# Kernel optimization log

Measured on AMD Instinct MI355X. Metric: run time of the kernel, lower is better.

The kernel has to match this reference:

```python
import jax, jax.numpy as jnp
import numpy as np

EMBED_DIM = 1024
NUM_HEADS = 16
HEAD_DIM = EMBED_DIM // NUM_HEADS


def setup_inputs() -> dict:
    key = jax.random.key(0)
    ks = jax.random.split(key, 5)
    T, B, E = 2048, 2, EMBED_DIM
    s = 1.0 / np.sqrt(E)
    return {
        "x": jax.random.normal(ks[0], (T, B, E), jnp.float32),
        "wq": jax.random.normal(ks[1], (E, E), jnp.float32) * s,
        "bq": jnp.zeros((E,), jnp.float32),
        "wk": jax.random.normal(ks[2], (E, E), jnp.float32) * s,
        "bk": jnp.zeros((E,), jnp.float32),
        "wv": jax.random.normal(ks[3], (E, E), jnp.float32) * s,
        "bv": jnp.zeros((E,), jnp.float32),
        "wo": jax.random.normal(ks[4], (E, E), jnp.float32) * s,
        "bo": jnp.zeros((E,), jnp.float32),
    }


def reference(x, wq, bq, wk, bk, wv, bv, wo, bo):
    # x: [T, B, E] (Time x Batch x Channel), self-attention: query = key = value = x
    T, B, E = x.shape
    H, D = NUM_HEADS, HEAD_DIM
    scaling = D ** -0.5
    # Linear projections (torch Linear: y = x @ W.T + b)
    q = (jnp.einsum('tbe,fe->tbf', x, wq) + bq) * scaling
    k = jnp.einsum('tbe,fe->tbf', x, wk) + bk
    v = jnp.einsum('tbe,fe->tbf', x, wv) + bv
    # reshape to [B*H, T, D] equivalent -> use [B, H, T, D]
    q = q.reshape(T, B, H, D).transpose(1, 2, 0, 3)  # [B,H,T,D]
    k = k.reshape(T, B, H, D).transpose(1, 2, 0, 3)
    v = v.reshape(T, B, H, D).transpose(1, 2, 0, 3)
    # scores: [B,H,T,S], fp32 softmax
    scores = jnp.einsum('bhtd,bhsd->bhts', q, k)
    probs = jax.nn.softmax(scores.astype(jnp.float32), axis=-1).astype(x.dtype)
    attn = jnp.einsum('bhts,bhsd->bhtd', probs, v)  # [B,H,T,D]
    attn = attn.transpose(2, 0, 1, 3).reshape(T, B, E)
    out = jnp.einsum('tbe,fe->tbf', attn, wo) + bo
    return out
```

## Files before the change

### kernel.cpp

```cpp
#include <hip/hip_runtime.h>
#include <cstddef>
#include <cstdint>

#define T_DIM 2048
#define E_DIM 1024
#define M_DIM 4096

typedef __attribute__((ext_vector_type(8))) short short8;
typedef __attribute__((ext_vector_type(8))) _Float16 half8;
typedef __attribute__((ext_vector_type(4))) float f32x4;

__device__ __forceinline__ short f16_bits(float v) {
  return __builtin_bit_cast(short, (_Float16)v);
}
__device__ __forceinline__ unsigned int pk2(float a, float b) {
  return __builtin_bit_cast(unsigned int, __builtin_amdgcn_cvt_pkrtz(a, b));
}
__device__ __forceinline__ half8 h8(short8 s) { return __builtin_bit_cast(half8, s); }

__device__ __forceinline__ void gl_lds16(const short* g, const short* l) {
  __builtin_amdgcn_global_load_lds(
      (const __attribute__((address_space(1))) unsigned int*)g,
      (__attribute__((address_space(3))) unsigned int*)l, 16, 0, 0);
}

__global__ __launch_bounds__(256) void convert_all(
    const float* __restrict__ x, const float* __restrict__ wq,
    const float* __restrict__ wk, const float* __restrict__ wv,
    const float* __restrict__ wo,
    short* __restrict__ xh, short* __restrict__ wqh, short* __restrict__ wkh,
    short* __restrict__ wvh, short* __restrict__ woh)
{
  const int bid = blockIdx.x;
  const float* in; short* hi; int base;
  if (bid < 4096)      { in = x;  hi = xh;  base = 0;    }
  else if (bid < 5120) { in = wq; hi = wqh; base = 4096; }
  else if (bid < 6144) { in = wk; hi = wkh; base = 5120; }
  else if (bid < 7168) { in = wv; hi = wvh; base = 6144; }
  else                 { in = wo; hi = woh; base = 7168; }
  const int i = (bid - base) * 256 + threadIdx.x;
  float4 v = ((const float4*)in)[i];
  uint2 p;
  p.x = (unsigned short)f16_bits(v.x) | ((unsigned int)(unsigned short)f16_bits(v.y) << 16);
  p.y = (unsigned short)f16_bits(v.z) | ((unsigned int)(unsigned short)f16_bits(v.w) << 16);
  ((uint2*)hi)[i] = p;
}

__global__ __launch_bounds__(256) void gemm_qkv(
    const short* __restrict__ xh,
    const short* __restrict__ wqh, const short* __restrict__ wkh,
    const short* __restrict__ wvh,
    const float* __restrict__ bq, const float* __restrict__ bk,
    const float* __restrict__ bv,
    short* __restrict__ qo, short* __restrict__ ko, short* __restrict__ vto)
{
  __shared__ __align__(16) short Ah[128 * 32], Wh[128 * 32];
  const int tid = threadIdx.x;
  const int lane = tid & 63;
  const int w = tid >> 6;
  const int quad = lane >> 4;
  const int l15 = lane & 15;
  const int sel = blockIdx.x >> 3;
  const int n0 = (blockIdx.x & 7) * 128;
  const int m0 = blockIdx.y * 128;

  const short* wsel = sel == 0 ? wqh : sel == 1 ? wkh : wvh;
  const float* bias = sel == 0 ? bq : sel == 1 ? bk : bv;
  const float scale = sel == 0 ? 0.125f * 1.44269504088896f : 1.0f;

  const short* gsrc = (w < 2) ? xh : wsel;
  short* lbuf = (w < 2) ? Ah : Wh;
  const int rbase = (w < 2) ? m0 : n0;
  const int jb = (w & 1) * 4;
  const int lrow = lane >> 2;
  const int gphys = lane & 3;

  f32x4 zero = {0.f, 0.f, 0.f, 0.f};
  f32x4 acc[4][4];
#pragma unroll
  for (int i = 0; i < 4; ++i)
#pragma unroll
    for (int j = 0; j < 4; ++j) acc[i][j] = zero;

  const int wm = w & 1, wn = w >> 1;

  for (int k0 = 0; k0 < E_DIM; k0 += 32) {
    __syncthreads();
#pragma unroll
    for (int jj = 0; jj < 4; ++jj) {
      int j = jb + jj;
      int r = j * 16 + lrow;
      int gl = (gphys - (r >> 1)) & 3;
      gl_lds16(gsrc + (size_t)(rbase + r) * E_DIM + k0 + gl * 8, lbuf + j * 512);
    }
    __syncthreads();
    short8 ahf[4];
#pragma unroll
    for (int i = 0; i < 4; ++i) {
      int r = wm * 64 + i * 16 + l15;
      int idx = r * 32 + ((quad + (r >> 1)) & 3) * 8;
      ahf[i] = *(const short8*)&Ah[idx];
    }
#pragma unroll
    for (int j = 0; j < 4; ++j) {
      int r = wn * 64 + j * 16 + l15;
      int idx = r * 32 + ((quad + (r >> 1)) & 3) * 8;
      short8 bhf = *(const short8*)&Wh[idx];
#pragma unroll
      for (int i = 0; i < 4; ++i)
        acc[i][j] = __builtin_amdgcn_mfma_f32_16x16x32_f16(h8(ahf[i]), h8(bhf), acc[i][j], 0, 0, 0);
    }
  }

#pragma unroll
  for (int j = 0; j < 4; ++j) {
    const int gc = n0 + wn * 64 + j * 16 + l15;
    const float bb = bias[gc];
    const int h = gc >> 6, d = gc & 63;
#pragma unroll
    for (int i = 0; i < 4; ++i) {
#pragma unroll
      for (int reg = 0; reg < 4; ++reg) {
        const int gm = m0 + wm * 64 + i * 16 + quad * 4 + reg;
        const float val = (acc[i][j][reg] + bb) * scale;
        const int t = gm >> 1, b = gm & 1;
        if (sel < 2) {
          short* dst = sel == 0 ? qo : ko;
          dst[((size_t)(b * 16 + h) * T_DIM + t) * 64 + d] = f16_bits(val);
        } else {
          vto[((size_t)(b * 16 + h) * 64 + d) * T_DIM + t] = f16_bits(val);
        }
      }
    }
  }
}

__global__ __launch_bounds__(256) void gemm_out(
    const short* __restrict__ attn, const short* __restrict__ woh,
    const float* __restrict__ bo, float* __restrict__ out)
{
  __shared__ __align__(16) short Ah[128 * 32], Wh[128 * 32];
  const int tid = threadIdx.x;
  const int lane = tid & 63;
  const int w = tid >> 6;
  const int quad = lane >> 4;
  const int l15 = lane & 15;
  const int n0 = blockIdx.x * 128;
  const int m0 = blockIdx.y * 128;

  const short* gsrc = (w < 2) ? attn : woh;
  short* lbuf = (w < 2) ? Ah : Wh;
  const int rbase = (w < 2) ? m0 : n0;
  const int jb = (w & 1) * 4;
  const int lrow = lane >> 2;
  const int gphys = lane & 3;

  f32x4 zero = {0.f, 0.f, 0.f, 0.f};
  f32x4 acc[4][4];
#pragma unroll
  for (int i = 0; i < 4; ++i)
#pragma unroll
    for (int j = 0; j < 4; ++j) acc[i][j] = zero;

  const int wm = w & 1, wn = w >> 1;

  for (int k0 = 0; k0 < E_DIM; k0 += 32) {
    __syncthreads();
#pragma unroll
    for (int jj = 0; jj < 4; ++jj) {
      int j = jb + jj;
      int r = j * 16 + lrow;
      int gl = (gphys - (r >> 1)) & 3;
      gl_lds16(gsrc + (size_t)(rbase + r) * E_DIM + k0 + gl * 8, lbuf + j * 512);
    }
    __syncthreads();
    short8 ahf[4];
#pragma unroll
    for (int i = 0; i < 4; ++i) {
      int r = wm * 64 + i * 16 + l15;
      int idx = r * 32 + ((quad + (r >> 1)) & 3) * 8;
      ahf[i] = *(const short8*)&Ah[idx];
    }
#pragma unroll
    for (int j = 0; j < 4; ++j) {
      int r = wn * 64 + j * 16 + l15;
      int idx = r * 32 + ((quad + (r >> 1)) & 3) * 8;
      short8 bhf = *(const short8*)&Wh[idx];
#pragma unroll
      for (int i = 0; i < 4; ++i)
        acc[i][j] = __builtin_amdgcn_mfma_f32_16x16x32_f16(h8(ahf[i]), h8(bhf), acc[i][j], 0, 0, 0);
    }
  }

#pragma unroll
  for (int j = 0; j < 4; ++j) {
    const int gc = n0 + wn * 64 + j * 16 + l15;
    const float bb = bo[gc];
#pragma unroll
    for (int i = 0; i < 4; ++i)
#pragma unroll
      for (int reg = 0; reg < 4; ++reg) {
        const int gm = m0 + wm * 64 + i * 16 + quad * 4 + reg;
        out[(size_t)gm * E_DIM + gc] = acc[i][j][reg] + bb;
      }
  }
}

__global__ __launch_bounds__(256) void attn_mfma(
    const short* __restrict__ q, const short* __restrict__ k,
    const short* __restrict__ vt, short* __restrict__ attn)
{
  __shared__ __align__(16) short Qs[128 * 64], Ks[64 * 64], Vs[64 * 64], Ps[4 * 32 * 64];
  const int tid = threadIdx.x;
  const int lane = tid & 63;
  const int w = tid >> 6;
  const int quad = lane >> 4;
  const int l15 = lane & 15;
  const int bhid = blockIdx.y;
  const int b = bhid >> 4, h = bhid & 15;
  const int t0 = blockIdx.x * 128;

  const short* qb = q + (size_t)bhid * T_DIM * 64;
  const short* kb = k + (size_t)bhid * T_DIM * 64;
  const short* vb = vt + (size_t)bhid * 64 * T_DIM;

  const int lrow8 = lane >> 3;
  const int gph8 = lane & 7;

#pragma unroll
  for (int jj = 0; jj < 4; ++jj) {
    int j = w * 4 + jj;
    int r = j * 8 + lrow8;
    int gl = (gph8 - (r >> 1)) & 7;
    gl_lds16(qb + (size_t)(t0 + r) * 64 + gl * 8, Qs + j * 512);
  }

  f32x4 zero = {0.f, 0.f, 0.f, 0.f};
  f32x4 acc[2][4];
  float l_part[2] = {0.f, 0.f};
#pragma unroll
  for (int rb = 0; rb < 2; ++rb)
#pragma unroll
    for (int jd = 0; jd < 4; ++jd) acc[rb][jd] = zero;

  short8 qa[2][2];

  for (int s0 = 0; s0 < T_DIM; s0 += 64) {
    __syncthreads();
    {
      const short* sb = (w < 2) ? kb : vb;
      short* lb = (w < 2) ? Ks : Vs;
      const int jb = (w & 1) * 4;
#pragma unroll
      for (int jj = 0; jj < 4; ++jj) {
        int j = jb + jj;
        int r = j * 8 + lrow8;
        int gl = (gph8 - (r >> 1)) & 7;
        size_t goff = (w < 2) ? (size_t)(s0 + r) * 64 + gl * 8
                              : (size_t)r * T_DIM + s0 + gl * 8;
        gl_lds16(sb + goff, lb + j * 512);
      }
    }
    __syncthreads();

    if (s0 == 0) {
#pragma unroll
      for (int rb = 0; rb < 2; ++rb)
#pragma unroll
        for (int step = 0; step < 2; ++step) {
          int r = w * 32 + rb * 16 + l15;
          int idx = r * 64 + (((step * 4 + quad) + (r >> 1)) & 7) * 8;
          qa[rb][step] = *(const short8*)&Qs[idx];
        }
    }

    f32x4 sc[2][4];
#pragma unroll
    for (int rb = 0; rb < 2; ++rb)
#pragma unroll
      for (int j = 0; j < 4; ++j) sc[rb][j] = zero;
#pragma unroll
    for (int j = 0; j < 4; ++j) {
      short8 kf[2];
#pragma unroll
      for (int step = 0; step < 2; ++step) {
        int r = j * 16 + l15;
        int idx = r * 64 + (((step * 4 + quad) + (r >> 1)) & 7) * 8;
        kf[step] = *(const short8*)&Ks[idx];
      }
#pragma unroll
      for (int rb = 0; rb < 2; ++rb)
#pragma unroll
        for (int step = 0; step < 2; ++step)
          sc[rb][j] = __builtin_amdgcn_mfma_f32_16x16x32_f16(h8(kf[step]), h8(qa[rb][step]), sc[rb][j], 0, 0, 0);
    }

#pragma unroll
    for (int rb = 0; rb < 2; ++rb) {
      const int row = rb * 16 + l15;
      const int wbase = w * 2048 + row * 64;
#pragma unroll
      for (int j = 0; j < 4; ++j) {
        float p0 = __builtin_amdgcn_exp2f(sc[rb][j][0]);
        float p1 = __builtin_amdgcn_exp2f(sc[rb][j][1]);
        float p2 = __builtin_amdgcn_exp2f(sc[rb][j][2]);
        float p3 = __builtin_amdgcn_exp2f(sc[rb][j][3]);
        l_part[rb] += (p0 + p1) + (p2 + p3);
        const int g = 2 * j + (quad >> 1);
        const int gp = (g + (row & 7)) & 7;
        uint2 pw;
        pw.x = pk2(p0, p1);
        pw.y = pk2(p2, p3);
        *(uint2*)&Ps[wbase + gp * 8 + (quad & 1) * 4] = pw;
      }
    }

    short8 pb[2][2];
#pragma unroll
    for (int rb = 0; rb < 2; ++rb)
#pragma unroll
      for (int step = 0; step < 2; ++step) {
        int row = rb * 16 + l15;
        int g = step * 4 + quad;
        int gp = (g + (row & 7)) & 7;
        pb[rb][step] = *(const short8*)&Ps[w * 2048 + row * 64 + gp * 8];
      }
#pragma unroll
    for (int jd = 0; jd < 4; ++jd) {
      short8 vf[2];
#pragma unroll
      for (int step = 0; step < 2; ++step) {
        int r = jd * 16 + l15;
        int idx = r * 64 + (((step * 4 + quad) + (r >> 1)) & 7) * 8;
        vf[step] = *(const short8*)&Vs[idx];
      }
#pragma unroll
      for (int rb = 0; rb < 2; ++rb)
#pragma unroll
        for (int step = 0; step < 2; ++step)
          acc[rb][jd] = __builtin_amdgcn_mfma_f32_16x16x32_f16(h8(vf[step]), h8(pb[rb][step]), acc[rb][jd], 0, 0, 0);
    }
  }

#pragma unroll
  for (int rb = 0; rb < 2; ++rb) {
    float l = l_part[rb];
    l += __shfl_xor(l, 16);
    l += __shfl_xor(l, 32);
    const float inv = 1.f / l;
    const int t = t0 + w * 32 + rb * 16 + l15;
    const size_t mrow = (size_t)(t * 2 + b) * E_DIM;
#pragma unroll
    for (int jd = 0; jd < 4; ++jd) {
      uint2 ov;
      ov.x = pk2(acc[rb][jd][0] * inv, acc[rb][jd][1] * inv);
      ov.y = pk2(acc[rb][jd][2] * inv, acc[rb][jd][3] * inv);
      *(uint2*)&attn[mrow + h * 64 + jd * 16 + quad * 4] = ov;
    }
  }
}

extern "C" void kernel_launch(void* const* d_in, const int* in_sizes, int n_in,
                              void* d_out, int out_size, void* d_ws, size_t ws_size,
                              hipStream_t stream)
{
  const float* x  = (const float*)d_in[0];
  const float* wq = (const float*)d_in[1];
  const float* bq = (const float*)d_in[2];
  const float* wk = (const float*)d_in[3];
  const float* bk = (const float*)d_in[4];
  const float* wv = (const float*)d_in[5];
  const float* bv = (const float*)d_in[6];
  const float* wo = (const float*)d_in[7];
  const float* bo = (const float*)d_in[8];
  float* out = (float*)d_out;

  short* ws = (short*)d_ws;
  const size_t M4 = (size_t)M_DIM * E_DIM;
  const size_t M1 = (size_t)E_DIM * E_DIM;
  short* xh   = ws;
  short* wqh  = xh + M4;
  short* wkh  = wqh + M1;
  short* wvh  = wkh + M1;
  short* woh  = wvh + M1;
  short* qws  = woh + M1;
  short* kws  = qws + M4;
  short* vtws = kws + M4;
  short* aws  = vtws + M4;

  convert_all<<<8192, 256, 0, stream>>>(x, wq, wk, wv, wo, xh, wqh, wkh, wvh, woh);
  gemm_qkv<<<dim3(24, 32), 256, 0, stream>>>(xh, wqh, wkh, wvh, bq, bk, bv,
                                             qws, kws, vtws);
  attn_mfma<<<dim3(16, 32), 256, 0, stream>>>(qws, kws, vtws, aws);
  gemm_out<<<dim3(8, 32), 256, 0, stream>>>(aws, woh, bo, out);
}
```

Before: 207.8 us.

## Double-buffer K/V in attention, split keys across waves, coalesce V transpose stores

The attention kernel now double-buffers K/V tiles in LDS, so the next chunk's global-to-LDS loads are issued while the current chunk is computed. Each wave now takes 16 keys against all 128 queries instead of 32 queries against all keys, so probabilities are exchanged through LDS (reusing the Q buffer) and row sums are reduced across waves at the end. Launch bounds ask for 3 blocks per CU. The QKV GEMM epilogue for V stages tiles through LDS so the transposed V output is written as 16-byte vectors instead of scattered 2-byte stores, at the cost of extra barriers and more register pressure from holding all Q fragments.

```diff
diff --git a/kernel.cpp b/kernel.cpp
--- a/kernel.cpp
+++ b/kernel.cpp
@@ -54,7 +54,9 @@
     const float* __restrict__ bv,
     short* __restrict__ qo, short* __restrict__ ko, short* __restrict__ vto)
 {
-  __shared__ __align__(16) short Ah[128 * 32], Wh[128 * 32];
+  __shared__ __align__(16) short smem[128 * 32 * 2];
+  short* Ah = smem;
+  short* Wh = smem + 128 * 32;
   const int tid = threadIdx.x;
   const int lane = tid & 63;
   const int w = tid >> 6;
@@ -112,24 +114,58 @@
     }
   }
 
-#pragma unroll
-  for (int j = 0; j < 4; ++j) {
-    const int gc = n0 + wn * 64 + j * 16 + l15;
-    const float bb = bias[gc];
-    const int h = gc >> 6, d = gc & 63;
-#pragma unroll
-    for (int i = 0; i < 4; ++i) {
-#pragma unroll
-      for (int reg = 0; reg < 4; ++reg) {
-        const int gm = m0 + wm * 64 + i * 16 + quad * 4 + reg;
-        const float val = (acc[i][j][reg] + bb) * scale;
-        const int t = gm >> 1, b = gm & 1;
-        if (sel < 2) {
-          short* dst = sel == 0 ? qo : ko;
+  if (sel < 2) {
+#pragma unroll
+    for (int j = 0; j < 4; ++j) {
+      const int gc = n0 + wn * 64 + j * 16 + l15;
+      const float bb = bias[gc];
+      const int h = gc >> 6, d = gc & 63;
+      short* dst = sel == 0 ? qo : ko;
+#pragma unroll
+      for (int i = 0; i < 4; ++i)
+#pragma unroll
+        for (int reg = 0; reg < 4; ++reg) {
+          const int gm = m0 + wm * 64 + i * 16 + quad * 4 + reg;
+          const float val = (acc[i][j][reg] + bb) * scale;
+          const int t = gm >> 1, b = gm & 1;
           dst[((size_t)(b * 16 + h) * T_DIM + t) * 64 + d] = f16_bits(val);
-        } else {
-          vto[((size_t)(b * 16 + h) * 64 + d) * T_DIM + t] = f16_bits(val);
         }
+    }
+  } else {
+    short* Tb = smem;
+    const int by = blockIdx.y;
+#pragma unroll
+    for (int R = 0; R < 2; ++R) {
+      __syncthreads();
+      if (wn == R) {
+#pragma unroll
+        for (int j = 0; j < 4; ++j) {
+          const int nl = j * 16 + l15;
+          const int gc = n0 + R * 64 + nl;
+          const float bb = bias[gc];
+#pragma unroll
+          for (int i = 0; i < 4; ++i) {
+            const int tp = wm * 32 + i * 8 + quad * 2;
+            unsigned int lo = pk2(acc[i][j][0] + bb, acc[i][j][2] + bb);
+            unsigned int hi = pk2(acc[i][j][1] + bb, acc[i][j][3] + bb);
+            const int g0 = tp >> 3;
+            const int sub = tp & 7;
+            *(unsigned int*)&Tb[nl * 128 + ((g0 + nl) & 15) * 8 + sub] = lo;
+            *(unsigned int*)&Tb[nl * 128 + ((g0 + 8 + nl) & 15) * 8 + sub] = hi;
+          }
+        }
+      }
+      __syncthreads();
+#pragma unroll
+      for (int ii = 0; ii < 4; ++ii) {
+        const int n = w * 16 + ii * 4 + quad;
+        const int g = (l15 - n) & 15;
+        short8 vvec = *(const short8*)&Tb[n * 128 + l15 * 8];
+        const int gc = n0 + R * 64 + n;
+        const int h = gc >> 6, d = gc & 63;
+        const int b = g >> 3;
+        const int t = by * 64 + (g & 7) * 8;
+        *(short8*)&vto[((size_t)(b * 16 + h) * 64 + d) * T_DIM + t] = vvec;
       }
     }
   }
@@ -206,11 +242,14 @@
   }
 }
 
-__global__ __launch_bounds__(256) void attn_mfma(
+__global__ __launch_bounds__(256, 3) void attn_mfma(
     const short* __restrict__ q, const short* __restrict__ k,
     const short* __restrict__ vt, short* __restrict__ attn)
 {
-  __shared__ __align__(16) short Qs[128 * 64], Ks[64 * 64], Vs[64 * 64], Ps[4 * 32 * 64];
+  __shared__ __align__(16) short QP[128 * 64];
+  __shared__ __align__(16) short Ks[2][64 * 64], Vs[2][64 * 64];
+  __shared__ float l_lds[4][128];
+
   const int tid = threadIdx.x;
   const int lane = tid & 63;
   const int w = tid >> 6;
@@ -232,130 +271,125 @@
     int j = w * 4 + jj;
     int r = j * 8 + lrow8;
     int gl = (gph8 - (r >> 1)) & 7;
-    gl_lds16(qb + (size_t)(t0 + r) * 64 + gl * 8, Qs + j * 512);
-  }
+    gl_lds16(qb + (size_t)(t0 + r) * 64 + gl * 8, QP + j * 512);
+  }
+#pragma unroll
+  for (int jj = 0; jj < 2; ++jj) {
+    int j = w * 2 + jj;
+    int r = j * 8 + lrow8;
+    int gl = (gph8 - (r >> 1)) & 7;
+    gl_lds16(kb + (size_t)r * 64 + gl * 8, Ks[0] + j * 512);
+    gl_lds16(vb + (size_t)r * T_DIM + 0 + gl * 8, Vs[0] + j * 512);
+  }
+  __syncthreads();
+
+  short8 qa[8][2];
+#pragma unroll
+  for (int qbk = 0; qbk < 8; ++qbk)
+#pragma unroll
+    for (int st = 0; st < 2; ++st) {
+      int r = qbk * 16 + l15;
+      int idx = r * 64 + (((st * 4 + quad) + (r >> 1)) & 7) * 8;
+      qa[qbk][st] = *(const short8*)&QP[idx];
+    }
+  __syncthreads();
 
   f32x4 zero = {0.f, 0.f, 0.f, 0.f};
-  f32x4 acc[2][4];
-  float l_part[2] = {0.f, 0.f};
-#pragma unroll
-  for (int rb = 0; rb < 2; ++rb)
-#pragma unroll
-    for (int jd = 0; jd < 4; ++jd) acc[rb][jd] = zero;
-
-  short8 qa[2][2];
-
-  for (int s0 = 0; s0 < T_DIM; s0 += 64) {
-    __syncthreads();
-    {
-      const short* sb = (w < 2) ? kb : vb;
-      short* lb = (w < 2) ? Ks : Vs;
-      const int jb = (w & 1) * 4;
-#pragma unroll
-      for (int jj = 0; jj < 4; ++jj) {
-        int j = jb + jj;
+  f32x4 acc[4][2];
+  float l_part[8];
+#pragma unroll
+  for (int d = 0; d < 4; ++d) { acc[d][0] = zero; acc[d][1] = zero; }
+#pragma unroll
+  for (int i = 0; i < 8; ++i) l_part[i] = 0.f;
+
+  for (int c = 0; c < 32; ++c) {
+    const int cur = c & 1;
+    if (c < 31) {
+      const int s0n = (c + 1) * 64;
+#pragma unroll
+      for (int jj = 0; jj < 2; ++jj) {
+        int j = w * 2 + jj;
         int r = j * 8 + lrow8;
         int gl = (gph8 - (r >> 1)) & 7;
-        size_t goff = (w < 2) ? (size_t)(s0 + r) * 64 + gl * 8
-                              : (size_t)r * T_DIM + s0 + gl * 8;
-        gl_lds16(sb + goff, lb + j * 512);
-      }
-    }
-    __syncthreads();
-
-    if (s0 == 0) {
-#pragma unroll
-      for (int rb = 0; rb < 2; ++rb)
-#pragma unroll
-        for (int step = 0; step < 2; ++step) {
-          int r = w * 32 + rb * 16 + l15;
-          int idx = r * 64 + (((step * 4 + quad) + (r >> 1)) & 7) * 8;
-          qa[rb][step] = *(const short8*)&Qs[idx];
-        }
-    }
-
-    f32x4 sc[2][4];
-#pragma unroll
-    for (int rb = 0; rb < 2; ++rb)
-#pragma unroll
-      for (int j = 0; j < 4; ++j) sc[rb][j] = zero;
-#pragma unroll
-    for (int j = 0; j < 4; ++j) {
-      short8 kf[2];
-#pragma unroll
-      for (int step = 0; step < 2; ++step) {
-        int r = j * 16 + l15;
-        int idx = r * 64 + (((step * 4 + quad) + (r >> 1)) & 7) * 8;
-        kf[step] = *(const short8*)&Ks[idx];
-      }
-#pragma unroll
-      for (int rb = 0; rb < 2; ++rb)
-#pragma unroll
-        for (int step = 0; step < 2; ++step)
-          sc[rb][j] = __builtin_amdgcn_mfma_f32_16x16x32_f16(h8(kf[step]), h8(qa[rb][step]), sc[rb][j], 0, 0, 0);
-    }
-
-#pragma unroll
-    for (int rb = 0; rb < 2; ++rb) {
-      const int row = rb * 16 + l15;
-      const int wbase = w * 2048 + row * 64;
-#pragma unroll
-      for (int j = 0; j < 4; ++j) {
-        float p0 = __builtin_amdgcn_exp2f(sc[rb][j][0]);
-        float p1 = __builtin_amdgcn_exp2f(sc[rb][j][1]);
-        float p2 = __builtin_amdgcn_exp2f(sc[rb][j][2]);
-        float p3 = __builtin_amdgcn_exp2f(sc[rb][j][3]);
-        l_part[rb] += (p0 + p1) + (p2 + p3);
-        const int g = 2 * j + (quad >> 1);
-        const int gp = (g + (row & 7)) & 7;
-        uint2 pw;
-        pw.x = pk2(p0, p1);
-        pw.y = pk2(p2, p3);
-        *(uint2*)&Ps[wbase + gp * 8 + (quad & 1) * 4] = pw;
-      }
-    }
+        gl_lds16(kb + (size_t)(s0n + r) * 64 + gl * 8, Ks[cur ^ 1] + j * 512);
+        gl_lds16(vb + (size_t)r * T_DIM + s0n + gl * 8, Vs[cur ^ 1] + j * 512);
+      }
+    }
+
+    short8 kf[2];
+#pragma unroll
+    for (int st = 0; st < 2; ++st) {
+      int r = w * 16 + l15;
+      int idx = r * 64 + (((st * 4 + quad) + (r >> 1)) & 7) * 8;
+      kf[st] = *(const short8*)&Ks[cur][idx];
+    }
+#pragma unroll
+    for (int qbk = 0; qbk < 8; ++qbk) {
+      f32x4 s = zero;
+      s = __builtin_amdgcn_mfma_f32_16x16x32_f16(h8(kf[0]), h8(qa[qbk][0]), s, 0, 0, 0);
+      s = __builtin_amdgcn_mfma_f32_16x16x32_f16(h8(kf[1]), h8(qa[qbk][1]), s, 0, 0, 0);
+      float p0 = __builtin_amdgcn_exp2f(s[0]);
+      float p1 = __builtin_amdgcn_exp2f(s[1]);
+      float p2 = __builtin_amdgcn_exp2f(s[2]);
+      float p3 = __builtin_amdgcn_exp2f(s[3]);
+      l_part[qbk] += (p0 + p1) + (p2 + p3);
+      const int qq = qbk * 16 + l15;
+      const int g = w * 2 + (quad >> 1);
+      const int gp = (g + (qq >> 1)) & 7;
+      uint2 pw; pw.x = pk2(p0, p1); pw.y = pk2(p2, p3);
+      *(uint2*)&QP[qq * 64 + gp * 8 + (quad & 1) * 4] = pw;
+    }
+    __syncthreads();
 
     short8 pb[2][2];
 #pragma unroll
-    for (int rb = 0; rb < 2; ++rb)
-#pragma unroll
-      for (int step = 0; step < 2; ++step) {
-        int row = rb * 16 + l15;
-        int g = step * 4 + quad;
-        int gp = (g + (row & 7)) & 7;
-        pb[rb][step] = *(const short8*)&Ps[w * 2048 + row * 64 + gp * 8];
-      }
-#pragma unroll
-    for (int jd = 0; jd < 4; ++jd) {
+    for (int qb2 = 0; qb2 < 2; ++qb2)
+#pragma unroll
+      for (int st = 0; st < 2; ++st) {
+        int qq = w * 32 + qb2 * 16 + l15;
+        int idx = qq * 64 + (((st * 4 + quad) + (qq >> 1)) & 7) * 8;
+        pb[qb2][st] = *(const short8*)&QP[idx];
+      }
+#pragma unroll
+    for (int dblk = 0; dblk < 4; ++dblk) {
       short8 vf[2];
 #pragma unroll
-      for (int step = 0; step < 2; ++step) {
-        int r = jd * 16 + l15;
-        int idx = r * 64 + (((step * 4 + quad) + (r >> 1)) & 7) * 8;
-        vf[step] = *(const short8*)&Vs[idx];
-      }
-#pragma unroll
-      for (int rb = 0; rb < 2; ++rb)
-#pragma unroll
-        for (int step = 0; step < 2; ++step)
-          acc[rb][jd] = __builtin_amdgcn_mfma_f32_16x16x32_f16(h8(vf[step]), h8(pb[rb][step]), acc[rb][jd], 0, 0, 0);
-    }
-  }
-
-#pragma unroll
-  for (int rb = 0; rb < 2; ++rb) {
-    float l = l_part[rb];
+      for (int st = 0; st < 2; ++st) {
+        int r = dblk * 16 + l15;
+        int idx = r * 64 + (((st * 4 + quad) + (r >> 1)) & 7) * 8;
+        vf[st] = *(const short8*)&Vs[cur][idx];
+      }
+#pragma unroll
+      for (int qb2 = 0; qb2 < 2; ++qb2) {
+        acc[dblk][qb2] = __builtin_amdgcn_mfma_f32_16x16x32_f16(h8(vf[0]), h8(pb[qb2][0]), acc[dblk][qb2], 0, 0, 0);
+        acc[dblk][qb2] = __builtin_amdgcn_mfma_f32_16x16x32_f16(h8(vf[1]), h8(pb[qb2][1]), acc[dblk][qb2], 0, 0, 0);
+      }
+    }
+    __syncthreads();
+  }
+
+#pragma unroll
+  for (int qbk = 0; qbk < 8; ++qbk) {
+    float l = l_part[qbk];
     l += __shfl_xor(l, 16);
     l += __shfl_xor(l, 32);
-    const float inv = 1.f / l;
-    const int t = t0 + w * 32 + rb * 16 + l15;
+    if (quad == 0) l_lds[w][qbk * 16 + l15] = l;
+  }
+  __syncthreads();
+
+#pragma unroll
+  for (int qb2 = 0; qb2 < 2; ++qb2) {
+    const int qq = w * 32 + qb2 * 16 + l15;
+    const float lsum = l_lds[0][qq] + l_lds[1][qq] + l_lds[2][qq] + l_lds[3][qq];
+    const float inv = 1.f / lsum;
+    const int t = t0 + qq;
     const size_t mrow = (size_t)(t * 2 + b) * E_DIM;
 #pragma unroll
-    for (int jd = 0; jd < 4; ++jd) {
+    for (int dblk = 0; dblk < 4; ++dblk) {
       uint2 ov;
-      ov.x = pk2(acc[rb][jd][0] * inv, acc[rb][jd][1] * inv);
-      ov.y = pk2(acc[rb][jd][2] * inv, acc[rb][jd][3] * inv);
-      *(uint2*)&attn[mrow + h * 64 + jd * 16 + quad * 4] = ov;
+      ov.x = pk2(acc[dblk][qb2][0] * inv, acc[dblk][qb2][1] * inv);
+      ov.y = pk2(acc[dblk][qb2][2] * inv, acc[dblk][qb2][3] * inv);
+      *(uint2*)&attn[mrow + h * 64 + dblk * 16 + quad * 4] = ov;
     }
   }
 }
```

New measurement: 206.0 us. Within noise of the previous version (-0.9%).
